# Kernel optimization log

Measured on AMD Instinct MI355X. Metric: run time of the kernel, lower is better.

## Reference

```python
import jax, jax.numpy as jnp
import numpy as np

N_NODES = 50000


def setup_inputs() -> dict:
    key = jax.random.key(0)
    ks = jax.random.split(key, 16)
    f = lambda k, shape: jax.random.normal(k, shape, dtype=jnp.float32) * 0.05
    ri = lambda k, shape: jax.random.randint(k, shape, 0, N_NODES, dtype=jnp.int32)
    return {
        "x": jax.random.normal(ks[0], (N_NODES, 128), dtype=jnp.float32),
        "W1": f(ks[1], (4, 128, 128)),
        "b1": f(ks[2], (4, 128)),
        "W2": f(ks[3], (4, 128, 128)),
        "b2": f(ks[4], (4, 128)),
        "P1w": f(ks[5], (128, 128)),
        "P1b": f(ks[6], (128,)),
        "P2w": f(ks[7], (128, 2)),
        "P2b": f(ks[8], (2,)),
        "src": ri(ks[9], (4, 200000)),
        "dst": ri(ks[10], (4, 200000)),
        "pos_src": ri(ks[11], (4, 200000)),
        "pos_dst": ri(ks[12], (4, 200000)),
        "neg_src": ri(ks[13], (4, 200000)),
        "neg_dst": ri(ks[14], (4, 200000)),
    }


def _hetero_conv(h, src, dst, W, b):
    """One HeteroGraphConv layer: per-relation GraphConv(norm='right'), no activation.

    h: [N, F_in]; src/dst: [R, E]; W: [R, F_in, F_out]; b: [R, F_out].
    Returns per-relation outputs [R, N, F_out] (caller applies activation then sums).
    """
    # sum of source features into destination nodes, per relation
    agg = jax.vmap(lambda s, d: jax.ops.segment_sum(h[s], d, num_segments=N_NODES))(src, dst)  # [R,N,Fin]
    deg = jax.vmap(lambda d: jax.ops.segment_sum(jnp.ones(d.shape, jnp.float32), d, num_segments=N_NODES))(dst)  # [R,N]
    norm = jnp.where(deg > 0, 1.0 / jnp.maximum(deg, 1.0), 0.0)[..., None]  # norm='right': 1/in_degree
    return jnp.einsum("rnf,rfo->rno", agg * norm, W) + b[:, None, :]


def _edge_scores(h, e_src, e_dst, P1w, P1b, P2w, P2b):
    # h[src]*h[dst] -> Linear -> ReLU -> Linear -> softmax -> class-1 prob
    e = h[e_src] * h[e_dst]  # [R,E,F]
    z = jax.nn.relu(jnp.einsum("ref,fo->reo", e, P1w) + P1b)
    logits = jnp.einsum("reo,oc->rec", z, P2w) + P2b
    return jax.nn.softmax(logits, axis=-1)[..., 1]  # [R,E]


def reference(x, W1, b1, W2, b2, P1w, P1b, P2w, P2b,
              src, dst, pos_src, pos_dst, neg_src, neg_dst):
    # Layer 1: relu per relation conv, then HeteroGraphConv sum across relations
    h = jnp.sum(jax.nn.relu(_hetero_conv(x, src, dst, W1, b1)), axis=0)  # [N, hidden]
    # Layer 2: no activation, sum across relations
    h = jnp.sum(_hetero_conv(h, src, dst, W2, b2), axis=0)  # [N, out]
    pos = _edge_scores(h, pos_src, pos_dst, P1w, P1b, P2w, P2b)
    neg = _edge_scores(h, neg_src, neg_dst, P1w, P1b, P2w, P2b)
    return (pos, neg)
```

## Files before the change

### kernel.cpp

```cpp
#include <hip/hip_runtime.h>
#include <hip/hip_bf16.h>
#include <math.h>

#define N_NODES 50000
#define N_EDGES 200000
#define N_REL   4
#define FDIM    128
#define SCAN_BLKS 49

typedef __attribute__((ext_vector_type(8))) short short8;
typedef __attribute__((ext_vector_type(4))) float f32x4;

static __device__ __forceinline__ ushort f2bf(float f) {
  union { float f; unsigned u; } v; v.f = f;
  unsigned r = v.u + 0x7fff + ((v.u >> 16) & 1);
  return (ushort)(r >> 16);
}
static __device__ __forceinline__ unsigned pk2(float lo, float hi) {
  __hip_bfloat162 t = __float22bfloat162_rn(make_float2(lo, hi));
  union { __hip_bfloat162 b; unsigned u; } v; v.b = t;
  return v.u;
}
static __device__ __forceinline__ float lo2f(unsigned u) {
  union { unsigned u; float f; } v; v.u = u << 16; return v.f;
}
static __device__ __forceinline__ float hi2f(unsigned u) {
  union { unsigned u; float f; } v; v.u = u & 0xffff0000u; return v.f;
}

__global__ void cnt_kernel(const int* __restrict__ dst, int* __restrict__ cnt) {
  int i = blockIdx.x * 256 + threadIdx.x;
  if (i < N_REL * N_EDGES) {
    int r = i / N_EDGES;
    atomicAdd(&cnt[r * N_NODES + dst[i]], 1);
  }
}

__global__ __launch_bounds__(1024) void scanA_kernel(
    const int* __restrict__ cnt, int* __restrict__ rowp,
    float* __restrict__ nrm, int* __restrict__ bsum) {
  int r = blockIdx.y, bx = blockIdx.x, t = threadIdx.x;
  int n = bx * 1024 + t;
  int g = r * N_NODES + n;
  int c = 0;
  if (n < N_NODES) {
    c = cnt[g];
    nrm[g] = c > 0 ? 1.f / (float)c : 0.f;
  }
  __shared__ int ts[1024];
  ts[t] = c;
  __syncthreads();
  for (int off = 1; off < 1024; off <<= 1) {
    int v = 0;
    if (t >= off) v = ts[t - off];
    __syncthreads();
    ts[t] += v;
    __syncthreads();
  }
  if (n < N_NODES) rowp[g] = ts[t] - c;
  if (t == 1023) bsum[r * SCAN_BLKS + bx] = ts[t];
}

__global__ void scanB_kernel(int* __restrict__ bsum) {
  int r = threadIdx.x;
  if (r < N_REL) {
    int run = r * N_EDGES;
    for (int b = 0; b < SCAN_BLKS; ++b) {
      int t = bsum[r * SCAN_BLKS + b];
      bsum[r * SCAN_BLKS + b] = run;
      run += t;
    }
  }
}

__global__ void scanC_kernel(int* __restrict__ rowp, int* __restrict__ cursor,
                             const int* __restrict__ bsum) {
  int i = blockIdx.x * 256 + threadIdx.x;
  if (i < N_REL * N_NODES) {
    int r = i / N_NODES;
    int n = i - r * N_NODES;
    int v = rowp[i] + bsum[r * SCAN_BLKS + (n >> 10)];
    rowp[i] = v;
    cursor[i] = v;
  }
}

__global__ void fill_kernel(const int* __restrict__ src, const int* __restrict__ dst,
                            int* __restrict__ cursor, int* __restrict__ csr_s) {
  int i = blockIdx.x * 256 + threadIdx.x;
  if (i < N_REL * N_EDGES) {
    int r = i / N_EDGES;
    int pos = atomicAdd(&cursor[r * N_NODES + dst[i]], 1);
    csr_s[pos] = src[i];
  }
}

__global__ void prep_all_kernel(const float* __restrict__ x, ushort* __restrict__ xb,
                                const float* __restrict__ P1w, ushort* __restrict__ bT,
                                const float* __restrict__ W1, ushort* __restrict__ wT1,
                                const float* __restrict__ W2, ushort* __restrict__ wT2) {
  const int NC = N_NODES * FDIM / 4;
  int i = blockIdx.x * 256 + threadIdx.x;
  if (i < NC) {
    float4 v = ((const float4*)x)[i];
    ((uint2*)xb)[i] = make_uint2(pk2(v.x, v.y), pk2(v.z, v.w));
    return;
  }
  int i2 = i - NC;
  if (i2 < FDIM * FDIM) {
    int c = i2 >> 7, k = i2 & 127;
    bT[i2] = f2bf(P1w[k * FDIM + c]);
    return;
  }
  i2 -= FDIM * FDIM;
  if (i2 < N_REL * FDIM * FDIM) {
    int r = i2 >> 14, c = (i2 >> 7) & 127, k = i2 & 127;
    wT1[i2] = f2bf(W1[(r << 14) + (k << 7) + c]);
    return;
  }
  i2 -= N_REL * FDIM * FDIM;
  if (i2 < N_REL * FDIM * FDIM) {
    int r = i2 >> 14, c = (i2 >> 7) & 127, k = i2 & 127;
    wT2[i2] = f2bf(W2[(r << 14) + (k << 7) + c]);
  }
}

__global__ __launch_bounds__(256) void conv_part_kernel(
    const ushort* __restrict__ hin, const int* __restrict__ rowp,
    const int* __restrict__ cnt, const float* __restrict__ nrm,
    const int* __restrict__ csr_s, const ushort* __restrict__ wT,
    const float* __restrict__ bias, ushort* __restrict__ hpart, int do_relu) {
  __shared__ __align__(16) short elds[64 * 128];
  __shared__ float nrm_lds[64];
  int tid  = threadIdx.x;
  int wave = tid >> 6, lane = tid & 63;
  int base = blockIdx.x * 64;
  int r    = blockIdx.y;
  int ig = tid >> 4, l16 = tid & 15;

  if (tid < 64) {
    int n = base + tid;
    nrm_lds[tid] = (n < N_NODES) ? nrm[r * N_NODES + n] : 0.f;
  }

  for (int rr = ig; rr < 64; rr += 16) {
    int n = base + rr;
    float a8[8];
#pragma unroll
    for (int q = 0; q < 8; ++q) a8[q] = 0.f;
    if (n < N_NODES) {
      int idx = r * N_NODES + n;
      int beg = rowp[idx], num = cnt[idx];
      int j = 0;
      for (; j + 4 <= num; j += 4) {
        int s0 = csr_s[beg + j], s1 = csr_s[beg + j + 1];
        int s2 = csr_s[beg + j + 2], s3 = csr_s[beg + j + 3];
        uint4 v0 = *(const uint4*)(hin + (size_t)s0 * FDIM + l16 * 8);
        uint4 v1 = *(const uint4*)(hin + (size_t)s1 * FDIM + l16 * 8);
        uint4 v2 = *(const uint4*)(hin + (size_t)s2 * FDIM + l16 * 8);
        uint4 v3 = *(const uint4*)(hin + (size_t)s3 * FDIM + l16 * 8);
        a8[0] += lo2f(v0.x) + lo2f(v1.x) + lo2f(v2.x) + lo2f(v3.x);
        a8[1] += hi2f(v0.x) + hi2f(v1.x) + hi2f(v2.x) + hi2f(v3.x);
        a8[2] += lo2f(v0.y) + lo2f(v1.y) + lo2f(v2.y) + lo2f(v3.y);
        a8[3] += hi2f(v0.y) + hi2f(v1.y) + hi2f(v2.y) + hi2f(v3.y);
        a8[4] += lo2f(v0.z) + lo2f(v1.z) + lo2f(v2.z) + lo2f(v3.z);
        a8[5] += hi2f(v0.z) + hi2f(v1.z) + hi2f(v2.z) + hi2f(v3.z);
        a8[6] += lo2f(v0.w) + lo2f(v1.w) + lo2f(v2.w) + lo2f(v3.w);
        a8[7] += hi2f(v0.w) + hi2f(v1.w) + hi2f(v2.w) + hi2f(v3.w);
      }
      for (; j < num; ++j) {
        int s = csr_s[beg + j];
        uint4 v = *(const uint4*)(hin + (size_t)s * FDIM + l16 * 8);
        a8[0] += lo2f(v.x); a8[1] += hi2f(v.x);
        a8[2] += lo2f(v.y); a8[3] += hi2f(v.y);
        a8[4] += lo2f(v.z); a8[5] += hi2f(v.z);
        a8[6] += lo2f(v.w); a8[7] += hi2f(v.w);
      }
    }
    int byte = rr * 256 + l16 * 16;
    byte ^= (rr & 7) << 4;
    *(uint4*)((char*)elds + byte) =
        make_uint4(pk2(a8[0], a8[1]), pk2(a8[2], a8[3]),
                   pk2(a8[4], a8[5]), pk2(a8[6], a8[7]));
  }
  __syncthreads();

  short8 bfrag[2][4];
#pragma unroll
  for (int t2 = 0; t2 < 2; ++t2) {
    int c = wave * 32 + t2 * 16 + (lane & 15);
#pragma unroll
    for (int k0 = 0; k0 < 4; ++k0)
      bfrag[t2][k0] = *(const short8*)(wT + ((size_t)r * FDIM + c) * FDIM + k0 * 32 + (lane >> 4) * 8);
  }

  ushort* hp = hpart + (size_t)r * N_NODES * FDIM;
#pragma unroll
  for (int tr = 0; tr < 4; ++tr) {
    int arow = tr * 16 + (lane & 15);
    short8 afrag[4];
#pragma unroll
    for (int k0 = 0; k0 < 4; ++k0) {
      int byte = arow * 256 + k0 * 64 + (lane >> 4) * 16;
      byte ^= (arow & 7) << 4;
      afrag[k0] = *(const short8*)((const char*)elds + byte);
    }
#pragma unroll
    for (int t2 = 0; t2 < 2; ++t2) {
      f32x4 acc = {0.f, 0.f, 0.f, 0.f};
#pragma unroll
      for (int k0 = 0; k0 < 4; ++k0)
        acc = __builtin_amdgcn_mfma_f32_16x16x32_bf16(afrag[k0], bfrag[t2][k0], acc, 0, 0, 0);
      int col = wave * 32 + t2 * 16 + (lane & 15);
      float bv = bias[r * FDIM + col];
#pragma unroll
      for (int j2 = 0; j2 < 4; ++j2) {
        int n = base + tr * 16 + (lane >> 4) * 4 + j2;
        if (n < N_NODES) {
          float nr = nrm_lds[tr * 16 + (lane >> 4) * 4 + j2];
          float v = acc[j2] * nr + bv;
          if (do_relu) v = fmaxf(v, 0.f);
          hp[(size_t)n * FDIM + col] = f2bf(v);
        }
      }
    }
  }
}

__global__ void finalize_kernel(const ushort* __restrict__ hpart, ushort* __restrict__ hout) {
  int i = blockIdx.x * 256 + threadIdx.x;
  const int NV = N_NODES * FDIM / 8;
  if (i < NV) {
    uint4 a = ((const uint4*)hpart)[i];
    uint4 b = ((const uint4*)(hpart + (size_t)N_NODES * FDIM))[i];
    uint4 c = ((const uint4*)(hpart + (size_t)2 * N_NODES * FDIM))[i];
    uint4 d = ((const uint4*)(hpart + (size_t)3 * N_NODES * FDIM))[i];
    float s0 = lo2f(a.x) + lo2f(b.x) + lo2f(c.x) + lo2f(d.x);
    float s1 = hi2f(a.x) + hi2f(b.x) + hi2f(c.x) + hi2f(d.x);
    float s2 = lo2f(a.y) + lo2f(b.y) + lo2f(c.y) + lo2f(d.y);
    float s3 = hi2f(a.y) + hi2f(b.y) + hi2f(c.y) + hi2f(d.y);
    float s4 = lo2f(a.z) + lo2f(b.z) + lo2f(c.z) + lo2f(d.z);
    float s5 = hi2f(a.z) + hi2f(b.z) + hi2f(c.z) + hi2f(d.z);
    float s6 = lo2f(a.w) + lo2f(b.w) + lo2f(c.w) + lo2f(d.w);
    float s7 = hi2f(a.w) + hi2f(b.w) + hi2f(c.w) + hi2f(d.w);
    ((uint4*)hout)[i] = make_uint4(pk2(s0, s1), pk2(s2, s3), pk2(s4, s5), pk2(s6, s7));
  }
}

__global__ __launch_bounds__(256) void edge_mfma_kernel(
    const ushort* __restrict__ hb,
    const int* __restrict__ psrc, const int* __restrict__ pdst,
    const int* __restrict__ nsrc, const int* __restrict__ ndst,
    const ushort* __restrict__ bT, const float* __restrict__ P1b,
    const float* __restrict__ P2w, const float* __restrict__ P2b,
    float* __restrict__ out) {
  __shared__ __align__(16) short elds[64 * 128];
  __shared__ float partials[4][128];

  int tid  = threadIdx.x;
  int wave = tid >> 6, lane = tid & 63;
  int b = blockIdx.x;
  const int HALF = (N_REL * N_EDGES) / 128;
  const int *esrc, *edst;
  float* o;
  int base;
  if (b < HALF) {
    esrc = psrc; edst = pdst; o = out; base = b * 128;
  } else {
    esrc = nsrc; edst = ndst; o = out + (size_t)N_REL * N_EDGES;
    base = (b - HALF) * 128;
  }

  int c0 = (2 * wave) * 16 + (lane & 15);
  int c1 = c0 + 16;
  float bz0 = P1b[c0], bz1 = P1b[c1];
  float wd0 = P2w[c0 * 2 + 1] - P2w[c0 * 2];
  float wd1 = P2w[c1 * 2 + 1] - P2w[c1 * 2];
  float cdiff = P2b[1] - P2b[0];

  short8 bfrag[2][4];
#pragma unroll
  for (int t2 = 0; t2 < 2; ++t2) {
    int c = (2 * wave + t2) * 16 + (lane & 15);
#pragma unroll
    for (int k0 = 0; k0 < 4; ++k0)
      bfrag[t2][k0] = *(const short8*)(bT + (size_t)c * 128 + k0 * 32 + (lane >> 4) * 8);
  }

  uint4 av0[4], gv0[4], av1[4], gv1[4];
#pragma unroll
  for (int j = 0; j < 4; ++j) {
    int flat = j * 256 + tid;
    int row = flat >> 4, f8 = flat & 15;
    int ge = base + row;
    int s = esrc[ge], d = edst[ge];
    av0[j] = *(const uint4*)(hb + (size_t)s * FDIM + f8 * 8);
    gv0[j] = *(const uint4*)(hb + (size_t)d * FDIM + f8 * 8);
  }
#pragma unroll
  for (int j = 0; j < 4; ++j) {
    int flat = j * 256 + tid;
    int row = flat >> 4, f8 = flat & 15;
    int ge = base + 64 + row;
    int s = esrc[ge], d = edst[ge];
    av1[j] = *(const uint4*)(hb + (size_t)s * FDIM + f8 * 8);
    gv1[j] = *(const uint4*)(hb + (size_t)d * FDIM + f8 * 8);
  }

  float part0[4][4], part1[4][4];
#pragma unroll
  for (int tr = 0; tr < 4; ++tr)
#pragma unroll
    for (int j2 = 0; j2 < 4; ++j2) { part0[tr][j2] = 0.f; part1[tr][j2] = 0.f; }

#pragma unroll
  for (int j = 0; j < 4; ++j) {
    int flat = j * 256 + tid;
    int row = flat >> 4, f8 = flat & 15;
    unsigned w0 = pk2(lo2f(av0[j].x) * lo2f(gv0[j].x), hi2f(av0[j].x) * hi2f(gv0[j].x));
    unsigned w1 = pk2(lo2f(av0[j].y) * lo2f(gv0[j].y), hi2f(av0[j].y) * hi2f(gv0[j].y));
    unsigned w2 = pk2(lo2f(av0[j].z) * lo2f(gv0[j].z), hi2f(av0[j].z) * hi2f(gv0[j].z));
    unsigned w3 = pk2(lo2f(av0[j].w) * lo2f(gv0[j].w), hi2f(av0[j].w) * hi2f(gv0[j].w));
    int byte = row * 256 + f8 * 16;
    byte ^= (row & 7) << 4;
    *(uint4*)((char*)elds + byte) = make_uint4(w0, w1, w2, w3);
  }
  __syncthreads();

#pragma unroll
  for (int tr = 0; tr < 4; ++tr) {
    int arow = tr * 16 + (lane & 15);
    short8 afrag[4];
#pragma unroll
    for (int k0 = 0; k0 < 4; ++k0) {
      int byte = arow * 256 + k0 * 64 + (lane >> 4) * 16;
      byte ^= (arow & 7) << 4;
      afrag[k0] = *(const short8*)((const char*)elds + byte);
    }
#pragma unroll
    for (int t2 = 0; t2 < 2; ++t2) {
      f32x4 acc = {0.f, 0.f, 0.f, 0.f};
#pragma unroll
      for (int k0 = 0; k0 < 4; ++k0)
        acc = __builtin_amdgcn_mfma_f32_16x16x32_bf16(afrag[k0], bfrag[t2][k0], acc, 0, 0, 0);
      float bz = t2 ? bz1 : bz0;
      float wdv = t2 ? wd1 : wd0;
#pragma unroll
      for (int j2 = 0; j2 < 4; ++j2)
        part0[tr][j2] += fmaxf(acc[j2] + bz, 0.f) * wdv;
    }
  }
  __syncthreads();

#pragma unroll
  for (int j = 0; j < 4; ++j) {
    int flat = j * 256 + tid;
    int row = flat >> 4, f8 = flat & 15;
    unsigned w0 = pk2(lo2f(av1[j].x) * lo2f(gv1[j].x), hi2f(av1[j].x) * hi2f(gv1[j].x));
    unsigned w1 = pk2(lo2f(av1[j].y) * lo2f(gv1[j].y), hi2f(av1[j].y) * hi2f(gv1[j].y));
    unsigned w2 = pk2(lo2f(av1[j].z) * lo2f(gv1[j].z), hi2f(av1[j].z) * hi2f(gv1[j].z));
    unsigned w3 = pk2(lo2f(av1[j].w) * lo2f(gv1[j].w), hi2f(av1[j].w) * hi2f(gv1[j].w));
    int byte = row * 256 + f8 * 16;
    byte ^= (row & 7) << 4;
    *(uint4*)((char*)elds + byte) = make_uint4(w0, w1, w2, w3);
  }
  __syncthreads();

#pragma unroll
  for (int tr = 0; tr < 4; ++tr) {
    int arow = tr * 16 + (lane & 15);
    short8 afrag[4];
#pragma unroll
    for (int k0 = 0; k0 < 4; ++k0) {
      int byte = arow * 256 + k0 * 64 + (lane >> 4) * 16;
      byte ^= (arow & 7) << 4;
      afrag[k0] = *(const short8*)((const char*)elds + byte);
    }
#pragma unroll
    for (int t2 = 0; t2 < 2; ++t2) {
      f32x4 acc = {0.f, 0.f, 0.f, 0.f};
#pragma unroll
      for (int k0 = 0; k0 < 4; ++k0)
        acc = __builtin_amdgcn_mfma_f32_16x16x32_bf16(afrag[k0], bfrag[t2][k0], acc, 0, 0, 0);
      float bz = t2 ? bz1 : bz0;
      float wdv = t2 ? wd1 : wd0;
#pragma unroll
      for (int j2 = 0; j2 < 4; ++j2)
        part1[tr][j2] += fmaxf(acc[j2] + bz, 0.f) * wdv;
    }
  }

#pragma unroll
  for (int tr = 0; tr < 4; ++tr)
#pragma unroll
    for (int j2 = 0; j2 < 4; ++j2) {
      float v = part0[tr][j2];
      v += __shfl_xor(v, 1);
      v += __shfl_xor(v, 2);
      v += __shfl_xor(v, 4);
      v += __shfl_xor(v, 8);
      float u = part1[tr][j2];
      u += __shfl_xor(u, 1);
      u += __shfl_xor(u, 2);
      u += __shfl_xor(u, 4);
      u += __shfl_xor(u, 8);
      if ((lane & 15) == 0) {
        int rowi = tr * 16 + (lane >> 4) * 4 + j2;
        partials[wave][rowi] = v;
        partials[wave][64 + rowi] = u;
      }
    }
  __syncthreads();

  if (tid < 128) {
    float s2 = partials[0][tid] + partials[1][tid] + partials[2][tid] + partials[3][tid] + cdiff;
    o[base + tid] = 1.f / (1.f + expf(-s2));
  }
}

extern "C" void kernel_launch(void* const* d_in, const int* in_sizes, int n_in,
                              void* d_out, int out_size, void* d_ws, size_t ws_size,
                              hipStream_t stream) {
  const float* x   = (const float*)d_in[0];
  const float* W1  = (const float*)d_in[1];
  const float* b1  = (const float*)d_in[2];
  const float* W2  = (const float*)d_in[3];
  const float* b2  = (const float*)d_in[4];
  const float* P1w = (const float*)d_in[5];
  const float* P1b = (const float*)d_in[6];
  const float* P2w = (const float*)d_in[7];
  const float* P2b = (const float*)d_in[8];
  const int* src     = (const int*)d_in[9];
  const int* dst     = (const int*)d_in[10];
  const int* pos_src = (const int*)d_in[11];
  const int* pos_dst = (const int*)d_in[12];
  const int* neg_src = (const int*)d_in[13];
  const int* neg_dst = (const int*)d_in[14];
  float* out = (float*)d_out;

  char* ws = (char*)d_ws;
  int*    cnt    = (int*)ws;     ws += (size_t)N_REL * N_NODES * 4;
  int*    rowp   = (int*)ws;     ws += (size_t)N_REL * N_NODES * 4;
  int*    cursor = (int*)ws;     ws += (size_t)N_REL * N_NODES * 4;
  int*    csr_s  = (int*)ws;     ws += (size_t)N_REL * N_EDGES * 4;
  float*  nrm    = (float*)ws;   ws += (size_t)N_REL * N_NODES * 4;
  int*    bsum   = (int*)ws;     ws += 4096;
  ushort* bT     = (ushort*)ws;  ws += (size_t)FDIM * FDIM * 2;
  ushort* wT1    = (ushort*)ws;  ws += (size_t)N_REL * FDIM * FDIM * 2;
  ushort* wT2    = (ushort*)ws;  ws += (size_t)N_REL * FDIM * FDIM * 2;
  ushort* xb     = (ushort*)ws;  ws += (size_t)N_NODES * FDIM * 2;
  ushort* h1b    = (ushort*)ws;  ws += (size_t)N_NODES * FDIM * 2;
  ushort* h2b    = (ushort*)ws;  ws += (size_t)N_NODES * FDIM * 2;
  ushort* hacc   = (ushort*)ws;

  hipMemsetAsync(cnt, 0, (size_t)N_REL * N_NODES * 4, stream);
  cnt_kernel<<<(N_REL * N_EDGES + 255) / 256, 256, 0, stream>>>(dst, cnt);
  scanA_kernel<<<dim3(SCAN_BLKS, N_REL), 1024, 0, stream>>>(cnt, rowp, nrm, bsum);
  scanB_kernel<<<1, 64, 0, stream>>>(bsum);
  scanC_kernel<<<(N_REL * N_NODES + 255) / 256, 256, 0, stream>>>(rowp, cursor, bsum);
  fill_kernel<<<(N_REL * N_EDGES + 255) / 256, 256, 0, stream>>>(src, dst, cursor, csr_s);
  {
    int total = N_NODES * FDIM / 4 + FDIM * FDIM + 2 * N_REL * FDIM * FDIM;
    prep_all_kernel<<<(total + 255) / 256, 256, 0, stream>>>(x, xb, P1w, bT, W1, wT1, W2, wT2);
  }

  conv_part_kernel<<<dim3((N_NODES + 63) / 64, N_REL), 256, 0, stream>>>(
      xb, rowp, cnt, nrm, csr_s, wT1, b1, hacc, 1);
  finalize_kernel<<<(N_NODES * FDIM / 8 + 255) / 256, 256, 0, stream>>>(hacc, h1b);
  conv_part_kernel<<<dim3((N_NODES + 63) / 64, N_REL), 256, 0, stream>>>(
      h1b, rowp, cnt, nrm, csr_s, wT2, b2, hacc, 0);
  finalize_kernel<<<(N_NODES * FDIM / 8 + 255) / 256, 256, 0, stream>>>(hacc, h2b);

  edge_mfma_kernel<<<2 * (N_REL * N_EDGES) / 128, 256, 0, stream>>>(
      h2b, pos_src, pos_dst, neg_src, neg_dst, bT, P1b, P2w, P2b, out);
}
```

Measured before the change: 464.6 us.

## Bucket scored edges by destination and remap blocks per XCD for L2 locality

```diff
diff --git a/kernel.cpp b/kernel.cpp
--- a/kernel.cpp
+++ b/kernel.cpp
@@ -7,6 +7,8 @@
 #define N_REL   4
 #define FDIM    128
 #define SCAN_BLKS 49
+#define E4 (N_REL * N_EDGES)
+#define NB 391
 
 typedef __attribute__((ext_vector_type(8))) short short8;
 typedef __attribute__((ext_vector_type(4))) float f32x4;
@@ -92,6 +94,49 @@
     int r = i / N_EDGES;
     int pos = atomicAdd(&cursor[r * N_NODES + dst[i]], 1);
     csr_s[pos] = src[i];
+  }
+}
+
+__global__ void ecnt_kernel(const int* __restrict__ pdst, const int* __restrict__ ndst,
+                            int* __restrict__ ec) {
+  int i = blockIdx.x * 256 + threadIdx.x;
+  if (i < 2 * E4) {
+    int side = i / E4, j = i - side * E4;
+    int d = side ? ndst[j] : pdst[j];
+    atomicAdd(&ec[side * NB + (d >> 7)], 1);
+  }
+}
+
+__global__ __launch_bounds__(512) void escan_kernel(const int* __restrict__ ec,
+                                                    int* __restrict__ ecur) {
+  int s = blockIdx.x, t = threadIdx.x;
+  __shared__ int ts[512];
+  int v = (t < NB) ? ec[s * NB + t] : 0;
+  ts[t] = v;
+  __syncthreads();
+  for (int off = 1; off < 512; off <<= 1) {
+    int u = 0;
+    if (t >= off) u = ts[t - off];
+    __syncthreads();
+    ts[t] += u;
+    __syncthreads();
+  }
+  if (t < NB) ecur[s * NB + t] = ts[t] - v + s * E4;
+}
+
+__global__ void efill_kernel(const int* __restrict__ psrc, const int* __restrict__ pdst,
+                             const int* __restrict__ nsrc, const int* __restrict__ ndst,
+                             int* __restrict__ ecur, int* __restrict__ s_src,
+                             int* __restrict__ s_dst, int* __restrict__ s_idx) {
+  int i = blockIdx.x * 256 + threadIdx.x;
+  if (i < 2 * E4) {
+    int side = i / E4, j = i - side * E4;
+    int sv = side ? nsrc[j] : psrc[j];
+    int dv = side ? ndst[j] : pdst[j];
+    int pos = atomicAdd(&ecur[side * NB + (dv >> 7)], 1);
+    s_src[pos] = sv;
+    s_dst[pos] = dv;
+    s_idx[pos] = side * E4 + j;
   }
 }
 
@@ -143,39 +188,47 @@
     nrm_lds[tid] = (n < N_NODES) ? nrm[r * N_NODES + n] : 0.f;
   }
 
-  for (int rr = ig; rr < 64; rr += 16) {
-    int n = base + rr;
+  int begs[4], nums[4];
+#pragma unroll
+  for (int q = 0; q < 4; ++q) {
+    int n = base + ig + 16 * q;
+    int ok = n < N_NODES;
+    int idx = r * N_NODES + (ok ? n : 0);
+    begs[q] = ok ? rowp[idx] : 0;
+    nums[q] = ok ? cnt[idx] : 0;
+  }
+
+#pragma unroll
+  for (int qi = 0; qi < 4; ++qi) {
+    int rr = ig + 16 * qi;
     float a8[8];
 #pragma unroll
     for (int q = 0; q < 8; ++q) a8[q] = 0.f;
-    if (n < N_NODES) {
-      int idx = r * N_NODES + n;
-      int beg = rowp[idx], num = cnt[idx];
-      int j = 0;
-      for (; j + 4 <= num; j += 4) {
-        int s0 = csr_s[beg + j], s1 = csr_s[beg + j + 1];
-        int s2 = csr_s[beg + j + 2], s3 = csr_s[beg + j + 3];
-        uint4 v0 = *(const uint4*)(hin + (size_t)s0 * FDIM + l16 * 8);
-        uint4 v1 = *(const uint4*)(hin + (size_t)s1 * FDIM + l16 * 8);
-        uint4 v2 = *(const uint4*)(hin + (size_t)s2 * FDIM + l16 * 8);
-        uint4 v3 = *(const uint4*)(hin + (size_t)s3 * FDIM + l16 * 8);
-        a8[0] += lo2f(v0.x) + lo2f(v1.x) + lo2f(v2.x) + lo2f(v3.x);
-        a8[1] += hi2f(v0.x) + hi2f(v1.x) + hi2f(v2.x) + hi2f(v3.x);
-        a8[2] += lo2f(v0.y) + lo2f(v1.y) + lo2f(v2.y) + lo2f(v3.y);
-        a8[3] += hi2f(v0.y) + hi2f(v1.y) + hi2f(v2.y) + hi2f(v3.y);
-        a8[4] += lo2f(v0.z) + lo2f(v1.z) + lo2f(v2.z) + lo2f(v3.z);
-        a8[5] += hi2f(v0.z) + hi2f(v1.z) + hi2f(v2.z) + hi2f(v3.z);
-        a8[6] += lo2f(v0.w) + lo2f(v1.w) + lo2f(v2.w) + lo2f(v3.w);
-        a8[7] += hi2f(v0.w) + hi2f(v1.w) + hi2f(v2.w) + hi2f(v3.w);
-      }
-      for (; j < num; ++j) {
-        int s = csr_s[beg + j];
-        uint4 v = *(const uint4*)(hin + (size_t)s * FDIM + l16 * 8);
-        a8[0] += lo2f(v.x); a8[1] += hi2f(v.x);
-        a8[2] += lo2f(v.y); a8[3] += hi2f(v.y);
-        a8[4] += lo2f(v.z); a8[5] += hi2f(v.z);
-        a8[6] += lo2f(v.w); a8[7] += hi2f(v.w);
-      }
+    int beg = begs[qi], num = nums[qi];
+    int j = 0;
+    for (; j + 4 <= num; j += 4) {
+      int s0 = csr_s[beg + j], s1 = csr_s[beg + j + 1];
+      int s2 = csr_s[beg + j + 2], s3 = csr_s[beg + j + 3];
+      uint4 v0 = *(const uint4*)(hin + (size_t)s0 * FDIM + l16 * 8);
+      uint4 v1 = *(const uint4*)(hin + (size_t)s1 * FDIM + l16 * 8);
+      uint4 v2 = *(const uint4*)(hin + (size_t)s2 * FDIM + l16 * 8);
+      uint4 v3 = *(const uint4*)(hin + (size_t)s3 * FDIM + l16 * 8);
+      a8[0] += lo2f(v0.x) + lo2f(v1.x) + lo2f(v2.x) + lo2f(v3.x);
+      a8[1] += hi2f(v0.x) + hi2f(v1.x) + hi2f(v2.x) + hi2f(v3.x);
+      a8[2] += lo2f(v0.y) + lo2f(v1.y) + lo2f(v2.y) + lo2f(v3.y);
+      a8[3] += hi2f(v0.y) + hi2f(v1.y) + hi2f(v2.y) + hi2f(v3.y);
+      a8[4] += lo2f(v0.z) + lo2f(v1.z) + lo2f(v2.z) + lo2f(v3.z);
+      a8[5] += hi2f(v0.z) + hi2f(v1.z) + hi2f(v2.z) + hi2f(v3.z);
+      a8[6] += lo2f(v0.w) + lo2f(v1.w) + lo2f(v2.w) + lo2f(v3.w);
+      a8[7] += hi2f(v0.w) + hi2f(v1.w) + hi2f(v2.w) + hi2f(v3.w);
+    }
+    for (; j < num; ++j) {
+      int s = csr_s[beg + j];
+      uint4 v = *(const uint4*)(hin + (size_t)s * FDIM + l16 * 8);
+      a8[0] += lo2f(v.x); a8[1] += hi2f(v.x);
+      a8[2] += lo2f(v.y); a8[3] += hi2f(v.y);
+      a8[4] += lo2f(v.z); a8[5] += hi2f(v.z);
+      a8[6] += lo2f(v.w); a8[7] += hi2f(v.w);
     }
     int byte = rr * 256 + l16 * 16;
     byte ^= (rr & 7) << 4;
@@ -249,8 +302,8 @@
 
 __global__ __launch_bounds__(256) void edge_mfma_kernel(
     const ushort* __restrict__ hb,
-    const int* __restrict__ psrc, const int* __restrict__ pdst,
-    const int* __restrict__ nsrc, const int* __restrict__ ndst,
+    const int* __restrict__ s_src, const int* __restrict__ s_dst,
+    const int* __restrict__ s_idx,
     const ushort* __restrict__ bT, const float* __restrict__ P1b,
     const float* __restrict__ P2w, const float* __restrict__ P2b,
     float* __restrict__ out) {
@@ -259,17 +312,13 @@
 
   int tid  = threadIdx.x;
   int wave = tid >> 6, lane = tid & 63;
-  int b = blockIdx.x;
-  const int HALF = (N_REL * N_EDGES) / 128;
-  const int *esrc, *edst;
-  float* o;
-  int base;
-  if (b < HALF) {
-    esrc = psrc; edst = pdst; o = out; base = b * 128;
-  } else {
-    esrc = nsrc; edst = ndst; o = out + (size_t)N_REL * N_EDGES;
-    base = (b - HALF) * 128;
-  }
+
+  const int NBLK = 2 * E4 / 128;
+  const int q = NBLK >> 3, r8 = NBLK & 7;
+  int b0 = blockIdx.x;
+  int xcd = b0 & 7, off = b0 >> 3;
+  int b = (xcd < r8 ? xcd * (q + 1) : r8 * (q + 1) + (xcd - r8) * q) + off;
+  int base = b * 128;
 
   int c0 = (2 * wave) * 16 + (lane & 15);
   int c1 = c0 + 16;
@@ -293,7 +342,7 @@
     int flat = j * 256 + tid;
     int row = flat >> 4, f8 = flat & 15;
     int ge = base + row;
-    int s = esrc[ge], d = edst[ge];
+    int s = s_src[ge], d = s_dst[ge];
     av0[j] = *(const uint4*)(hb + (size_t)s * FDIM + f8 * 8);
     gv0[j] = *(const uint4*)(hb + (size_t)d * FDIM + f8 * 8);
   }
@@ -302,7 +351,7 @@
     int flat = j * 256 + tid;
     int row = flat >> 4, f8 = flat & 15;
     int ge = base + 64 + row;
-    int s = esrc[ge], d = edst[ge];
+    int s = s_src[ge], d = s_dst[ge];
     av1[j] = *(const uint4*)(hb + (size_t)s * FDIM + f8 * 8);
     gv1[j] = *(const uint4*)(hb + (size_t)d * FDIM + f8 * 8);
   }
@@ -414,7 +463,7 @@
 
   if (tid < 128) {
     float s2 = partials[0][tid] + partials[1][tid] + partials[2][tid] + partials[3][tid] + cdiff;
-    o[base + tid] = 1.f / (1.f + expf(-s2));
+    out[s_idx[base + tid]] = 1.f / (1.f + expf(-s2));
   }
 }
 
@@ -445,6 +494,11 @@
   int*    csr_s  = (int*)ws;     ws += (size_t)N_REL * N_EDGES * 4;
   float*  nrm    = (float*)ws;   ws += (size_t)N_REL * N_NODES * 4;
   int*    bsum   = (int*)ws;     ws += 4096;
+  int*    ec     = (int*)ws;     ws += 4096;
+  int*    ecur   = (int*)ws;     ws += 4096;
+  int*    s_src  = (int*)ws;     ws += (size_t)2 * E4 * 4;
+  int*    s_dst  = (int*)ws;     ws += (size_t)2 * E4 * 4;
+  int*    s_idx  = (int*)ws;     ws += (size_t)2 * E4 * 4;
   ushort* bT     = (ushort*)ws;  ws += (size_t)FDIM * FDIM * 2;
   ushort* wT1    = (ushort*)ws;  ws += (size_t)N_REL * FDIM * FDIM * 2;
   ushort* wT2    = (ushort*)ws;  ws += (size_t)N_REL * FDIM * FDIM * 2;
@@ -454,11 +508,16 @@
   ushort* hacc   = (ushort*)ws;
 
   hipMemsetAsync(cnt, 0, (size_t)N_REL * N_NODES * 4, stream);
+  hipMemsetAsync(ec, 0, 4096, stream);
   cnt_kernel<<<(N_REL * N_EDGES + 255) / 256, 256, 0, stream>>>(dst, cnt);
+  ecnt_kernel<<<(2 * E4 + 255) / 256, 256, 0, stream>>>(pos_dst, neg_dst, ec);
   scanA_kernel<<<dim3(SCAN_BLKS, N_REL), 1024, 0, stream>>>(cnt, rowp, nrm, bsum);
   scanB_kernel<<<1, 64, 0, stream>>>(bsum);
+  escan_kernel<<<2, 512, 0, stream>>>(ec, ecur);
   scanC_kernel<<<(N_REL * N_NODES + 255) / 256, 256, 0, stream>>>(rowp, cursor, bsum);
   fill_kernel<<<(N_REL * N_EDGES + 255) / 256, 256, 0, stream>>>(src, dst, cursor, csr_s);
+  efill_kernel<<<(2 * E4 + 255) / 256, 256, 0, stream>>>(
+      pos_src, pos_dst, neg_src, neg_dst, ecur, s_src, s_dst, s_idx);
   {
     int total = N_NODES * FDIM / 4 + FDIM * FDIM + 2 * N_REL * FDIM * FDIM;
     prep_all_kernel<<<(total + 255) / 256, 256, 0, stream>>>(x, xb, P1w, bT, W1, wT1, W2, wT2);
@@ -471,6 +530,6 @@
       h1b, rowp, cnt, nrm, csr_s, wT2, b2, hacc, 0);
   finalize_kernel<<<(N_NODES * FDIM / 8 + 255) / 256, 256, 0, stream>>>(hacc, h2b);
 
-  edge_mfma_kernel<<<2 * (N_REL * N_EDGES) / 128, 256, 0, stream>>>(
-      h2b, pos_src, pos_dst, neg_src, neg_dst, bT, P1b, P2w, P2b, out);
-}
+  edge_mfma_kernel<<<2 * E4 / 128, 256, 0, stream>>>(
+      h2b, s_src, s_dst, s_idx, bT, P1b, P2w, P2b, out);
+}
```

After: 1.369 ms. 2.95x slower.
